# Performance work log

Hardware: AMD Instinct MI355X
Metric: run time of the kernel (lower is better)

Reference implementation:

```python
import jax, jax.numpy as jnp
import numpy as np

SEQ, BATCH, HIDDEN = 4096, 16, 512


def setup_inputs() -> dict:
    key = jax.random.key(0)
    ks = jax.random.split(key, 8)
    scale = 1.0 / np.sqrt(HIDDEN)
    outputs_hidden = jax.random.normal(ks[0], (1, BATCH, HIDDEN), jnp.float32)
    encoder_out = jax.random.normal(ks[1], (SEQ, BATCH, HIDDEN), jnp.float32)
    encoder_features = jax.random.normal(ks[2], (SEQ, BATCH, HIDDEN), jnp.float32)
    # binary-ish float mask, mostly ones
    encoder_mask = (jax.random.uniform(ks[3], (BATCH, 1, SEQ)) > 0.1).astype(jnp.float32)
    # running sum of positive exp-scores; keep strictly positive
    temporal_scores_sum = jax.random.uniform(ks[4], (BATCH, 1, SEQ)) + 0.5
    W_feat = jax.random.normal(ks[5], (HIDDEN, HIDDEN), jnp.float32) * scale
    b_feat = jax.random.normal(ks[6], (HIDDEN,), jnp.float32)
    v_attn = jax.random.normal(ks[7], (HIDDEN,), jnp.float32) * scale
    return {
        "outputs_hidden": outputs_hidden,
        "encoder_out": encoder_out,
        "encoder_features": encoder_features,
        "encoder_mask": encoder_mask,
        "temporal_scores_sum": temporal_scores_sum,
        "W_feat": W_feat,
        "b_feat": b_feat,
        "v_attn": v_attn,
    }


def reference(outputs_hidden, encoder_out, encoder_features, encoder_mask,
              temporal_scores_sum, W_feat, b_feat, v_attn):
    # self.features: Linear(hidden, hidden) on decoder state [1, b, h]
    decoder_features = jnp.einsum('obh,kh->obk', outputs_hidden, W_feat) + b_feat
    # additive score: tanh(dec + enc) . v  -> [s, b]
    scores = jnp.einsum('sbh,h->sb', jnp.tanh(decoder_features + encoder_features), v_attn)
    # Permute(1,2,0) of [s,b,1] -> [b,1,s], then exp
    temporal_attention = jnp.exp(scores).T[:, None, :]  # [b, 1, s]
    attention = temporal_attention / temporal_scores_sum
    new_scores_sum = temporal_attention + temporal_scores_sum
    attention = attention * encoder_mask
    attention = attention / jnp.sum(attention, axis=-1, keepdims=True)  # Normalize(-1)
    enc = jnp.transpose(encoder_out, (1, 0, 2))           # [b, s, h]
    context = jnp.matmul(attention, enc)                  # [b, 1, h]
    context = jnp.transpose(context, (1, 0, 2))           # [1, b, h]
    return context, attention, new_scores_sum
```

## Files before the change

### kernel.cpp

```cpp
#include <hip/hip_runtime.h>
#include <hip/hip_bf16.h>
#include <stdint.h>

#define SEQ 4096
#define BATCH 16
#define HID 512
#define ATT_OFF (BATCH * HID)
#define NSS_OFF (BATCH * HID + BATCH * SEQ)

typedef unsigned short u16;
typedef unsigned int u32;

__device__ __forceinline__ float bflo(u32 w) { return __uint_as_float(w << 16); }
__device__ __forceinline__ float bfhi(u32 w) { return __uint_as_float(w & 0xffff0000u); }

__device__ __forceinline__ u16 f2bf(float f) {
  u32 u = __float_as_uint(f);
  return (u16)((u + 0x7fffu + ((u >> 16) & 1u)) >> 16);
}

__device__ __forceinline__ int probe_bf16(const void* tssp) {
  const u16* t = (const u16*)tssp;
  int ok = 1;
  #pragma unroll
  for (int i = 0; i < 8; i += 2) {
    u16 u = t[i];
    ok &= (u >= 0x3F00 && u <= 0x3FC0) ? 1 : 0;
  }
  return ok;
}

template <int BF>
__device__ __forceinline__ float ld1(const void* p, size_t i) {
  if (BF) return __uint_as_float(((u32)((const u16*)p)[i]) << 16);
  return ((const float*)p)[i];
}

template <int BF>
__device__ __forceinline__ void st1(void* p, size_t i, float v) {
  if (BF) ((u16*)p)[i] = f2bf(v);
  else    ((float*)p)[i] = v;
}

template <int BF>
__device__ __forceinline__ void load8(const void* p, size_t e, float* o) {
  if (BF) {
    uint4 v = *(const uint4*)((const u16*)p + e);
    o[0]=bflo(v.x); o[1]=bfhi(v.x); o[2]=bflo(v.y); o[3]=bfhi(v.y);
    o[4]=bflo(v.z); o[5]=bfhi(v.z); o[6]=bflo(v.w); o[7]=bfhi(v.w);
  } else {
    const float4* f = (const float4*)((const float*)p + e);
    float4 a = f[0], b = f[1];
    o[0]=a.x; o[1]=a.y; o[2]=a.z; o[3]=a.w;
    o[4]=b.x; o[5]=b.y; o[6]=b.z; o[7]=b.w;
  }
}

__device__ __forceinline__ float fast_tanh(float x) {
  float e = __expf(2.0f * x);
  return 1.0f - 2.0f * __builtin_amdgcn_rcpf(e + 1.0f);
}

__device__ __forceinline__ float wave_sum(float acc) {
  #pragma unroll
  for (int off = 32; off; off >>= 1) acc += __shfl_xor(acc, off, 64);
  return acc;
}

template <int BF>
__device__ __forceinline__ void k_dec_body(
    const void* oh, const void* W, const void* bias, float* dec) {
  int tid = threadIdx.x;
  int gw = blockIdx.x * 4 + (tid >> 6);
  int lane = tid & 63;
  int k = gw & (HID - 1);
  int b = gw >> 9;
  float wv[8], ov[8];
  load8<BF>(W,  (size_t)k * HID + lane * 8, wv);
  load8<BF>(oh, (size_t)b * HID + lane * 8, ov);
  float acc = 0.0f;
  #pragma unroll
  for (int j = 0; j < 8; ++j) acc += wv[j] * ov[j];
  acc = wave_sum(acc);
  if (lane == 0) dec[b * HID + k] = acc + ld1<BF>(bias, k);
}

__global__ __launch_bounds__(256) void k_dec(
    const void* oh, const void* W, const void* bias, const void* tss,
    float* dec, float* denom) {
  if (blockIdx.x == 0 && threadIdx.x < BATCH) denom[threadIdx.x] = 0.0f;
  if (probe_bf16(tss)) k_dec_body<1>(oh, W, bias, dec);
  else                 k_dec_body<0>(oh, W, bias, dec);
}

template <int BF>
__device__ __forceinline__ void k_scores_body(
    const void* ef, const void* maskp, const void* tssp, const void* vp,
    const float* dec, float* w_out, float* denom, void* out) {
  int tid = threadIdx.x, lane = tid & 63, wave = tid >> 6;
  int blk = blockIdx.x;
  int b = blk >> 8;
  int s_base = (blk & 255) * 16;
  float dv[8], vv[8];
  #pragma unroll
  for (int j = 0; j < 8; ++j) dv[j] = dec[b * HID + lane * 8 + j];
  load8<BF>(vp, lane * 8, vv);
  __shared__ float wpart[16];
  #pragma unroll
  for (int i = 0; i < 4; ++i) {
    int s = s_base + wave * 4 + i;
    float ev[8];
    load8<BF>(ef, ((size_t)s * BATCH + b) * HID + lane * 8, ev);
    float acc = 0.0f;
    #pragma unroll
    for (int j = 0; j < 8; ++j) acc += fast_tanh(ev[j] + dv[j]) * vv[j];
    acc = wave_sum(acc);
    if (lane == 0) {
      float p  = __expf(acc);
      float ts = ld1<BF>(tssp,  b * SEQ + s);
      float m  = ld1<BF>(maskp, b * SEQ + s);
      float w  = p * m * __builtin_amdgcn_rcpf(ts);
      st1<BF>(out, NSS_OFF + b * SEQ + s, p + ts);
      w_out[b * SEQ + s] = w;
      wpart[wave * 4 + i] = w;
    }
  }
  __syncthreads();
  if (tid == 0) {
    float sum = 0.0f;
    #pragma unroll
    for (int j = 0; j < 16; ++j) sum += wpart[j];
    atomicAdd(&denom[b], sum);
  }
}

__global__ __launch_bounds__(256) void k_scores(
    const void* ef, const void* maskp, const void* tssp, const void* vp,
    const float* dec, float* w_out, float* denom, void* out) {
  if (probe_bf16(tssp)) k_scores_body<1>(ef, maskp, tssp, vp, dec, w_out, denom, out);
  else                  k_scores_body<0>(ef, maskp, tssp, vp, dec, w_out, denom, out);
}

#define K3_CHUNK 128
template <int BF>
__device__ __forceinline__ void k_context_body(
    const void* eo, const float* w, const float* denom,
    float* partial, void* out) {
  int blk = blockIdx.x;
  int b = blk >> 5;
  int chunk = blk & 31;
  int s0 = chunk * K3_CHUNK;
  int tid = threadIdx.x, lane = tid & 63, sg = tid >> 6;
  __shared__ float w_s[K3_CHUNK];
  __shared__ float red[192 * 8];
  float inv_d = __builtin_amdgcn_rcpf(denom[b]);
  if (tid < K3_CHUNK) {
    float wv = w[b * SEQ + s0 + tid];
    w_s[tid] = wv;
    st1<BF>(out, ATT_OFF + b * SEQ + s0 + tid, wv * inv_d);
  }
  __syncthreads();
  float a[8] = {0,0,0,0,0,0,0,0};
  #pragma unroll 4
  for (int i = 0; i < K3_CHUNK / 4; ++i) {
    int sl = 4 * i + sg;
    int s = s0 + sl;
    float ev[8];
    load8<BF>(eo, ((size_t)s * BATCH + b) * HID + lane * 8, ev);
    float ws = w_s[sl];
    #pragma unroll
    for (int j = 0; j < 8; ++j) a[j] += ws * ev[j];
  }
  if (sg > 0) {
    float* r = &red[(((sg - 1) * 64) + lane) * 8];
    #pragma unroll
    for (int j = 0; j < 8; ++j) r[j] = a[j];
  }
  __syncthreads();
  if (sg == 0) {
    #pragma unroll
    for (int k = 0; k < 3; ++k) {
      const float* r = &red[((k * 64) + lane) * 8];
      #pragma unroll
      for (int j = 0; j < 8; ++j) a[j] += r[j];
    }
    float4* p4 = (float4*)(partial + (size_t)chunk * (BATCH * HID) + b * HID + lane * 8);
    p4[0] = make_float4(a[0], a[1], a[2], a[3]);
    p4[1] = make_float4(a[4], a[5], a[6], a[7]);
  }
}

__global__ __launch_bounds__(256) void k_context(
    const void* eo, const float* w, const float* denom, const void* tssp,
    float* partial, void* out) {
  if (probe_bf16(tssp)) k_context_body<1>(eo, w, denom, partial, out);
  else                  k_context_body<0>(eo, w, denom, partial, out);
}

__global__ __launch_bounds__(256) void k_reduce_ctx(
    const float* __restrict__ partial, const float* __restrict__ denom,
    const void* tssp, void* out) {
  int idx = blockIdx.x * 256 + threadIdx.x;
  int b = idx >> 9;
  float sum = 0.0f;
  #pragma unroll
  for (int c = 0; c < 32; ++c) sum += partial[c * (BATCH * HID) + idx];
  float v = sum * __builtin_amdgcn_rcpf(denom[b]);
  if (probe_bf16(tssp)) st1<1>(out, idx, v);
  else                  st1<0>(out, idx, v);
}

extern "C" void kernel_launch(void* const* d_in, const int* in_sizes, int n_in,
                              void* d_out, int out_size, void* d_ws, size_t ws_size,
                              hipStream_t stream) {
  const void* oh   = d_in[0];
  const void* eo   = d_in[1];
  const void* ef   = d_in[2];
  const void* mask = d_in[3];
  const void* tss  = d_in[4];
  const void* W    = d_in[5];
  const void* bias = d_in[6];
  const void* v    = d_in[7];

  float* ws      = (float*)d_ws;
  float* dec     = ws;
  float* w_buf   = dec + BATCH * HID;
  float* denom   = w_buf + BATCH * SEQ;
  float* partial = denom + 16;

  k_dec       <<<2048, 256, 0, stream>>>(oh, W, bias, tss, dec, denom);
  k_scores    <<<4096, 256, 0, stream>>>(ef, mask, tss, v, dec, w_buf, denom, d_out);
  k_context   <<< 512, 256, 0, stream>>>(eo, w_buf, denom, tss, partial, d_out);
  k_reduce_ctx<<<  32, 256, 0, stream>>>(partial, denom, tss, d_out);
}
```

Before: 322.3 us.

## Restructure scores and context around per-position tiles and add probe pass

Scores blocks now cover 8 sequence positions across all batches, with decoder features staged in LDS. This replaces the per-batch blocks and the atomic denominator. Context blocks accumulate all batches for 8 positions into an LDS tile with shared-memory atomics and write 512 partial chunks. Separate kernels then compute the attention normalisation and the context reduction. A new k_probe kernel streams the whole encoder_features tensor into a scratch sum. That adds a full extra read, apparently as a bandwidth or cache experiment.

Result: slower. 383.7 us (+19.0%).

```diff
diff --git a/kernel.cpp b/kernel.cpp
--- a/kernel.cpp
+++ b/kernel.cpp
@@ -7,6 +7,7 @@
 #define HID 512
 #define ATT_OFF (BATCH * HID)
 #define NSS_OFF (BATCH * HID + BATCH * SEQ)
+#define NCH 512
 
 typedef unsigned short u16;
 typedef unsigned int u32;
@@ -61,10 +62,17 @@
   return 1.0f - 2.0f * __builtin_amdgcn_rcpf(e + 1.0f);
 }
 
-__device__ __forceinline__ float wave_sum(float acc) {
-  #pragma unroll
-  for (int off = 32; off; off >>= 1) acc += __shfl_xor(acc, off, 64);
-  return acc;
+__global__ __launch_bounds__(256) void k_probe(
+    const void* efv, const void* tssp, float* __restrict__ pout) {
+  const float4* ef = (const float4*)efv;
+  size_t g = (size_t)blockIdx.x * 256 + threadIdx.x;
+  int iters = probe_bf16(tssp) ? 8 : 16;
+  float acc = 0.0f;
+  for (int i = 0; i < iters; ++i) {
+    float4 v = ef[g + (size_t)i * 524288];
+    acc += v.x + v.y + v.z + v.w;
+  }
+  pout[g] = acc;
 }
 
 template <int BF>
@@ -81,14 +89,14 @@
   float acc = 0.0f;
   #pragma unroll
   for (int j = 0; j < 8; ++j) acc += wv[j] * ov[j];
-  acc = wave_sum(acc);
+  #pragma unroll
+  for (int off = 32; off; off >>= 1) acc += __shfl_xor(acc, off, 64);
   if (lane == 0) dec[b * HID + k] = acc + ld1<BF>(bias, k);
 }
 
 __global__ __launch_bounds__(256) void k_dec(
     const void* oh, const void* W, const void* bias, const void* tss,
-    float* dec, float* denom) {
-  if (blockIdx.x == 0 && threadIdx.x < BATCH) denom[threadIdx.x] = 0.0f;
+    float* dec) {
   if (probe_bf16(tss)) k_dec_body<1>(oh, W, bias, dec);
   else                 k_dec_body<0>(oh, W, bias, dec);
 }
@@ -96,118 +104,159 @@
 template <int BF>
 __device__ __forceinline__ void k_scores_body(
     const void* ef, const void* maskp, const void* tssp, const void* vp,
-    const float* dec, float* w_out, float* denom, void* out) {
+    const float* dec, float* w_buf, void* out) {
+  int tid = threadIdx.x, lane = tid & 63, wave = tid >> 6;
+  int s0 = blockIdx.x * 8;
+  __shared__ float dlds[BATCH * HID];
+  {
+    const float4* src = (const float4*)dec;
+    float4* dst = (float4*)dlds;
+    #pragma unroll
+    for (int i = 0; i < 8; ++i) dst[tid * 8 + i] = src[tid * 8 + i];
+  }
+  float vv[8];
+  load8<BF>(vp, lane * 8, vv);
+  __syncthreads();
+  #pragma unroll
+  for (int g = 0; g < 4; ++g) {
+    int s  = s0 + wave * 2 + (g >> 1);
+    int b0 = (g & 1) * 8;
+    float acc[8];
+    #pragma unroll
+    for (int i = 0; i < 8; ++i) {
+      float ev[8];
+      load8<BF>(ef, ((size_t)s * BATCH + b0 + i) * HID + lane * 8, ev);
+      const float4* dv4 = (const float4*)&dlds[(b0 + i) * HID + lane * 8];
+      float4 dA = dv4[0], dB = dv4[1];
+      float dv[8] = {dA.x, dA.y, dA.z, dA.w, dB.x, dB.y, dB.z, dB.w};
+      float a = 0.0f;
+      #pragma unroll
+      for (int j = 0; j < 8; ++j) a += fast_tanh(ev[j] + dv[j]) * vv[j];
+      acc[i] = a;
+    }
+    #pragma unroll
+    for (int off = 32; off; off >>= 1)
+      #pragma unroll
+      for (int i = 0; i < 8; ++i) acc[i] += __shfl_xor(acc[i], off, 64);
+    #pragma unroll
+    for (int i = 0; i < 8; ++i) {
+      int b = b0 + i;
+      float p  = __expf(acc[i]);
+      float ts = ld1<BF>(tssp,  (size_t)b * SEQ + s);
+      float m  = ld1<BF>(maskp, (size_t)b * SEQ + s);
+      float w  = p * m * __builtin_amdgcn_rcpf(ts);
+      if (lane == 0) {
+        st1<BF>(out, NSS_OFF + (size_t)b * SEQ + s, p + ts);
+        w_buf[(size_t)b * SEQ + s] = w;
+      }
+    }
+  }
+}
+
+__global__ __launch_bounds__(256) void k_scores(
+    const void* ef, const void* maskp, const void* tssp, const void* vp,
+    const float* dec, float* w_buf, void* out) {
+  if (probe_bf16(tssp)) k_scores_body<1>(ef, maskp, tssp, vp, dec, w_buf, out);
+  else                  k_scores_body<0>(ef, maskp, tssp, vp, dec, w_buf, out);
+}
+
+template <int BF>
+__device__ __forceinline__ void k_ctx_body(
+    const void* eo, const float* w_buf, float* partial) {
   int tid = threadIdx.x, lane = tid & 63, wave = tid >> 6;
   int blk = blockIdx.x;
-  int b = blk >> 8;
-  int s_base = (blk & 255) * 16;
-  float dv[8], vv[8];
-  #pragma unroll
-  for (int j = 0; j < 8; ++j) dv[j] = dec[b * HID + lane * 8 + j];
-  load8<BF>(vp, lane * 8, vv);
-  __shared__ float wpart[16];
-  #pragma unroll
-  for (int i = 0; i < 4; ++i) {
-    int s = s_base + wave * 4 + i;
-    float ev[8];
-    load8<BF>(ef, ((size_t)s * BATCH + b) * HID + lane * 8, ev);
-    float acc = 0.0f;
-    #pragma unroll
-    for (int j = 0; j < 8; ++j) acc += fast_tanh(ev[j] + dv[j]) * vv[j];
-    acc = wave_sum(acc);
-    if (lane == 0) {
-      float p  = __expf(acc);
-      float ts = ld1<BF>(tssp,  b * SEQ + s);
-      float m  = ld1<BF>(maskp, b * SEQ + s);
-      float w  = p * m * __builtin_amdgcn_rcpf(ts);
-      st1<BF>(out, NSS_OFF + b * SEQ + s, p + ts);
-      w_out[b * SEQ + s] = w;
-      wpart[wave * 4 + i] = w;
+  int s0 = blk * 8;
+  __shared__ float tile[BATCH * HID];
+  {
+    float4* t4 = (float4*)tile;
+    #pragma unroll
+    for (int i = 0; i < 8; ++i) t4[tid * 8 + i] = make_float4(0, 0, 0, 0);
+  }
+  __syncthreads();
+  int sA = s0 + wave * 2, sB = sA + 1;
+  #pragma unroll 2
+  for (int b = 0; b < BATCH; ++b) {
+    float wA = w_buf[(size_t)b * SEQ + sA];
+    float wB = w_buf[(size_t)b * SEQ + sB];
+    size_t rA = ((size_t)sA * BATCH + b) * HID;
+    size_t rB = ((size_t)sB * BATCH + b) * HID;
+    float a[8];
+    #pragma unroll
+    for (int k = 0; k < 8; ++k) {
+      float eA = ld1<BF>(eo, rA + lane + 64 * k);
+      float eB = ld1<BF>(eo, rB + lane + 64 * k);
+      a[k] = wA * eA + wB * eB;
     }
-  }
-  __syncthreads();
-  if (tid == 0) {
-    float sum = 0.0f;
-    #pragma unroll
-    for (int j = 0; j < 16; ++j) sum += wpart[j];
-    atomicAdd(&denom[b], sum);
-  }
-}
-
-__global__ __launch_bounds__(256) void k_scores(
-    const void* ef, const void* maskp, const void* tssp, const void* vp,
-    const float* dec, float* w_out, float* denom, void* out) {
-  if (probe_bf16(tssp)) k_scores_body<1>(ef, maskp, tssp, vp, dec, w_out, denom, out);
-  else                  k_scores_body<0>(ef, maskp, tssp, vp, dec, w_out, denom, out);
-}
-
-#define K3_CHUNK 128
-template <int BF>
-__device__ __forceinline__ void k_context_body(
-    const void* eo, const float* w, const float* denom,
-    float* partial, void* out) {
-  int blk = blockIdx.x;
-  int b = blk >> 5;
-  int chunk = blk & 31;
-  int s0 = chunk * K3_CHUNK;
-  int tid = threadIdx.x, lane = tid & 63, sg = tid >> 6;
-  __shared__ float w_s[K3_CHUNK];
-  __shared__ float red[192 * 8];
-  float inv_d = __builtin_amdgcn_rcpf(denom[b]);
-  if (tid < K3_CHUNK) {
-    float wv = w[b * SEQ + s0 + tid];
-    w_s[tid] = wv;
-    st1<BF>(out, ATT_OFF + b * SEQ + s0 + tid, wv * inv_d);
-  }
-  __syncthreads();
-  float a[8] = {0,0,0,0,0,0,0,0};
-  #pragma unroll 4
-  for (int i = 0; i < K3_CHUNK / 4; ++i) {
-    int sl = 4 * i + sg;
-    int s = s0 + sl;
-    float ev[8];
-    load8<BF>(eo, ((size_t)s * BATCH + b) * HID + lane * 8, ev);
-    float ws = w_s[sl];
-    #pragma unroll
-    for (int j = 0; j < 8; ++j) a[j] += ws * ev[j];
-  }
-  if (sg > 0) {
-    float* r = &red[(((sg - 1) * 64) + lane) * 8];
-    #pragma unroll
-    for (int j = 0; j < 8; ++j) r[j] = a[j];
-  }
-  __syncthreads();
-  if (sg == 0) {
-    #pragma unroll
-    for (int k = 0; k < 3; ++k) {
-      const float* r = &red[((k * 64) + lane) * 8];
-      #pragma unroll
-      for (int j = 0; j < 8; ++j) a[j] += r[j];
-    }
-    float4* p4 = (float4*)(partial + (size_t)chunk * (BATCH * HID) + b * HID + lane * 8);
-    p4[0] = make_float4(a[0], a[1], a[2], a[3]);
-    p4[1] = make_float4(a[4], a[5], a[6], a[7]);
-  }
-}
-
-__global__ __launch_bounds__(256) void k_context(
-    const void* eo, const float* w, const float* denom, const void* tssp,
-    float* partial, void* out) {
-  if (probe_bf16(tssp)) k_context_body<1>(eo, w, denom, partial, out);
-  else                  k_context_body<0>(eo, w, denom, partial, out);
-}
-
-__global__ __launch_bounds__(256) void k_reduce_ctx(
-    const float* __restrict__ partial, const float* __restrict__ denom,
-    const void* tssp, void* out) {
-  int idx = blockIdx.x * 256 + threadIdx.x;
-  int b = idx >> 9;
-  float sum = 0.0f;
-  #pragma unroll
-  for (int c = 0; c < 32; ++c) sum += partial[c * (BATCH * HID) + idx];
-  float v = sum * __builtin_amdgcn_rcpf(denom[b]);
-  if (probe_bf16(tssp)) st1<1>(out, idx, v);
-  else                  st1<0>(out, idx, v);
+    #pragma unroll
+    for (int k = 0; k < 8; ++k)
+      atomicAdd(&tile[b * HID + lane + 64 * k], a[k]);
+  }
+  __syncthreads();
+  #pragma unroll
+  for (int q = 0; q < 8; ++q) {
+    int fidx = (tid * 8 + q) * 4;
+    int b = fidx >> 9, h = fidx & 511;
+    *(float4*)(partial + ((size_t)b * NCH + blk) * HID + h) = *(float4*)(tile + fidx);
+  }
+}
+
+__global__ __launch_bounds__(256) void k_ctx(
+    const void* eo, const float* w_buf, const void* tssp, float* partial) {
+  if (probe_bf16(tssp)) k_ctx_body<1>(eo, w_buf, partial);
+  else                  k_ctx_body<0>(eo, w_buf, partial);
+}
+
+template <int BF>
+__device__ __forceinline__ void fin_att_body(
+    const float* w_buf, float* denom_ws, void* out) {
+  int b = blockIdx.x, t = threadIdx.x;
+  float wl[16];
+  float ps = 0.0f;
+  #pragma unroll
+  for (int k = 0; k < 16; ++k) {
+    wl[k] = w_buf[(size_t)b * SEQ + k * 256 + t];
+    ps += wl[k];
+  }
+  #pragma unroll
+  for (int off = 32; off; off >>= 1) ps += __shfl_xor(ps, off, 64);
+  __shared__ float r[4];
+  if ((t & 63) == 0) r[t >> 6] = ps;
+  __syncthreads();
+  float denom = r[0] + r[1] + r[2] + r[3];
+  float inv = __builtin_amdgcn_rcpf(denom);
+  if (t == 0) denom_ws[b] = denom;
+  #pragma unroll
+  for (int k = 0; k < 16; ++k)
+    st1<BF>(out, ATT_OFF + (size_t)b * SEQ + k * 256 + t, wl[k] * inv);
+}
+
+__global__ __launch_bounds__(256) void k_fin_att(
+    const float* w_buf, float* denom_ws, const void* tssp, void* out) {
+  if (probe_bf16(tssp)) fin_att_body<1>(w_buf, denom_ws, out);
+  else                  fin_att_body<0>(w_buf, denom_ws, out);
+}
+
+template <int BF>
+__device__ __forceinline__ void fin_ctx_body(
+    const float* partial, const float* denom_ws, void* out) {
+  int b = blockIdx.x >> 1;
+  int h = ((blockIdx.x & 1) << 8) + threadIdx.x;
+  const float* base = partial + (size_t)b * NCH * HID + h;
+  float a0 = 0, a1 = 0, a2 = 0, a3 = 0;
+  for (int c = 0; c < NCH; c += 4) {
+    a0 += base[(size_t)c * HID];
+    a1 += base[(size_t)(c + 1) * HID];
+    a2 += base[(size_t)(c + 2) * HID];
+    a3 += base[(size_t)(c + 3) * HID];
+  }
+  st1<BF>(out, (size_t)b * HID + h,
+          (a0 + a1 + a2 + a3) * __builtin_amdgcn_rcpf(denom_ws[b]));
+}
+
+__global__ __launch_bounds__(256) void k_fin_ctx(
+    const float* partial, const float* denom_ws, const void* tssp, void* out) {
+  if (probe_bf16(tssp)) fin_ctx_body<1>(partial, denom_ws, out);
+  else                  fin_ctx_body<0>(partial, denom_ws, out);
 }
 
 extern "C" void kernel_launch(void* const* d_in, const int* in_sizes, int n_in,
@@ -222,14 +271,17 @@
   const void* bias = d_in[6];
   const void* v    = d_in[7];
 
-  float* ws      = (float*)d_ws;
-  float* dec     = ws;
-  float* w_buf   = dec + BATCH * HID;
-  float* denom   = w_buf + BATCH * SEQ;
-  float* partial = denom + 16;
-
-  k_dec       <<<2048, 256, 0, stream>>>(oh, W, bias, tss, dec, denom);
-  k_scores    <<<4096, 256, 0, stream>>>(ef, mask, tss, v, dec, w_buf, denom, d_out);
-  k_context   <<< 512, 256, 0, stream>>>(eo, w_buf, denom, tss, partial, d_out);
-  k_reduce_ctx<<<  32, 256, 0, stream>>>(partial, denom, tss, d_out);
-}
+  float* ws       = (float*)d_ws;
+  float* dec      = ws;
+  float* w_buf    = dec + BATCH * HID;
+  float* denom_ws = w_buf + BATCH * SEQ;
+  float* partial  = denom_ws + 16;
+  float* probe_o  = partial + BATCH * NCH * HID;
+
+  k_probe  <<<2048, 256, 0, stream>>>(ef, tss, probe_o);
+  k_dec    <<<2048, 256, 0, stream>>>(oh, W, bias, tss, dec);
+  k_scores <<< 512, 256, 0, stream>>>(ef, mask, tss, v, dec, w_buf, d_out);
+  k_ctx    <<< 512, 256, 0, stream>>>(eo, w_buf, tss, partial);
+  k_fin_att<<<  16, 256, 0, stream>>>(w_buf, denom_ws, tss, d_out);
+  k_fin_ctx<<<  32, 256, 0, stream>>>(partial, denom_ws, tss, d_out);
+}
```
